# Kernel tuning notes

Measured on AMD Instinct MI355X. Metric: run time of the kernel, lower is better.

Reference implementation:

```python
import jax, jax.numpy as jnp
import numpy as np

BN_EPS = 1e-5


def setup_inputs() -> dict:
    key = jax.random.key(0)
    ks = jax.random.split(key, 12)
    N, K, C_IN, C_OUT = 50000, 16, 128, 128
    C2 = 2 * C_OUT
    return {
        "features": jax.random.normal(ks[0], (N, C_IN), dtype=jnp.float32),
        "neighbor_idx": jax.random.randint(ks[1], (N, K), 0, N, dtype=jnp.int64),
        "W1": jax.random.normal(ks[2], (C_IN, C2), dtype=jnp.float32) * 0.05,
        "b1": jax.random.normal(ks[3], (C2,), dtype=jnp.float32) * 0.05,
        "gamma": jax.random.uniform(ks[4], (C2,), dtype=jnp.float32, minval=0.5, maxval=1.5),
        "beta": jax.random.normal(ks[5], (C2,), dtype=jnp.float32) * 0.05,
        "run_mean": jax.random.normal(ks[6], (C2,), dtype=jnp.float32) * 0.05,
        "run_var": jax.random.uniform(ks[7], (C2,), dtype=jnp.float32, minval=0.5, maxval=1.5),
        "Ws": jax.random.normal(ks[8], (C2, C2), dtype=jnp.float32) * 0.05,
        "Wm": jax.random.normal(ks[9], (C2, C_OUT), dtype=jnp.float32) * 0.05,
        "bm": jax.random.normal(ks[10], (C_OUT,), dtype=jnp.float32) * 0.05,
    }


def reference(features, neighbor_idx, W1, b1, gamma, beta, run_mean, run_var, Ws, Wm, bm):
    # mlp1: Linear + ReLU (no BN)
    x = jax.nn.relu(features @ W1 + b1)                     # (N, 2C)
    # gather_neighbour: irregular index_select
    g = x[neighbor_idx]                                     # (N, k, 2C)
    # BatchNorm1d over channel dim (inference semantics, running stats)
    inv = gamma * jax.lax.rsqrt(run_var + BN_EPS)
    g = (g - run_mean) * inv + beta                         # (N, k, 2C)
    # AttentivePooling: per-neighbor score linear (no bias), softmax over k
    scores = jax.nn.softmax(g @ Ws, axis=1)                 # (N, k, 2C)
    feat = jnp.sum(scores * g, axis=1)                      # (N, 2C)
    return feat @ Wm + bm                                   # (N, C_out)
```

## Files before the change

kernel.cpp:

```cpp
#include <hip/hip_runtime.h>
#include <cstddef>

#define C_IN  128
#define C2    256
#define C_OUT 128
#define KNBR  16

typedef unsigned short u16;
typedef __attribute__((ext_vector_type(8))) short bf16x8;
typedef __attribute__((ext_vector_type(4))) float f32x4;

__device__ __forceinline__ float bf2f(u16 h) {
    return __uint_as_float(((unsigned int)h) << 16);
}
__device__ __forceinline__ u16 f2bf(float x) {
    unsigned int u = __float_as_uint(x);
    return (u16)((u + 0x7fffu + ((u >> 16) & 1u)) >> 16);
}

__global__ void prep_k(const float* __restrict__ W1, const float* __restrict__ Ws,
                       const float* __restrict__ Wm, u16* __restrict__ W1t,
                       u16* __restrict__ Wst, u16* __restrict__ Wmt)
{
    const int n = blockIdx.x, t = threadIdx.x;
    if (blockIdx.y == 0) {
        if (t < 128) W1t[n * 128 + t] = f2bf(W1[t * 256 + n]);
    } else if (blockIdx.y == 1) {
        Wst[n * 256 + t] = f2bf(Ws[t * 256 + n]);
    } else {
        if (n < 128) Wmt[n * 256 + t] = f2bf(Wm[t * 128 + n]);
    }
}

template<int MODE, bool A_BF16>
__global__ __launch_bounds__(256)
void mfma_gemm(const void* __restrict__ Ap, int lda,
               const u16* __restrict__ Bt,
               const float* __restrict__ bias, const float* __restrict__ gamma,
               const float* __restrict__ beta, const float* __restrict__ mean,
               const float* __restrict__ var,
               float* __restrict__ Cf, u16* __restrict__ packed,
               u16* __restrict__ xbn_c, int M, int Kd, int Nc)
{
    __shared__ u16 As[128][72];
    __shared__ u16 Bs[128][72];
    const int tid = threadIdx.x;
    const int w = tid >> 6, l = tid & 63, q = l >> 4, r = l & 15;
    const int wm = w & 1, wn = w >> 1;
    const int m0 = blockIdx.x * 128, n0 = blockIdx.y * 128;

    f32x4 acc[4][4] = {};

    for (int k0 = 0; k0 < Kd; k0 += 64) {
        if (A_BF16) {
            const u16* A = (const u16*)Ap;
            #pragma unroll
            for (int i = 0; i < 4; i++) {
                int idx = tid + i * 256;
                int row = idx >> 3, g = (idx & 7) * 8;
                int gm = m0 + row;
                uint4 v = make_uint4(0u, 0u, 0u, 0u);
                if (gm < M)
                    v = *(const uint4*)(A + (size_t)gm * lda + k0 + g);
                *(uint4*)&As[row][g] = v;
            }
        } else {
            const float* A = (const float*)Ap;
            #pragma unroll
            for (int i = 0; i < 8; i++) {
                int idx = tid + i * 256;
                int row = idx >> 4, g = (idx & 15) * 4;
                int gm = m0 + row;
                float4 v = make_float4(0.f, 0.f, 0.f, 0.f);
                if (gm < M)
                    v = *(const float4*)(A + (size_t)gm * lda + k0 + g);
                ushort4 h;
                h.x = f2bf(v.x); h.y = f2bf(v.y);
                h.z = f2bf(v.z); h.w = f2bf(v.w);
                *(ushort4*)&As[row][g] = h;
            }
        }
        #pragma unroll
        for (int i = 0; i < 4; i++) {
            int idx = tid + i * 256;
            int row = idx >> 3, g = (idx & 7) * 8;
            *(uint4*)&Bs[row][g] =
                *(const uint4*)(Bt + (size_t)(n0 + row) * Kd + k0 + g);
        }
        __syncthreads();

        #pragma unroll
        for (int h = 0; h < 2; h++) {
            bf16x8 af[4], bfr[4];
            #pragma unroll
            for (int i = 0; i < 4; i++)
                af[i] = *(const bf16x8*)&As[wm * 64 + i * 16 + r][h * 32 + q * 8];
            #pragma unroll
            for (int j = 0; j < 4; j++)
                bfr[j] = *(const bf16x8*)&Bs[wn * 64 + j * 16 + r][h * 32 + q * 8];
            #pragma unroll
            for (int i = 0; i < 4; i++)
                #pragma unroll
                for (int j = 0; j < 4; j++)
                    acc[i][j] = __builtin_amdgcn_mfma_f32_16x16x32_bf16(
                        af[i], bfr[j], acc[i][j], 0, 0, 0);
        }
        __syncthreads();
    }

    #pragma unroll
    for (int j = 0; j < 4; j++) {
        const int ch = n0 + wn * 64 + j * 16 + r;
        float bi = 0.f, be = 0.f, mu = 0.f, iv = 0.f, bo = 0.f;
        if (MODE == 1) {
            bi = bias[ch]; be = beta[ch]; mu = mean[ch];
            iv = gamma[ch] * rsqrtf(var[ch] + 1e-5f);
        }
        if (MODE == 2) bo = bias[ch];
        const int goff = (ch >> 2) * 8 + (ch & 3);
        #pragma unroll
        for (int i = 0; i < 4; i++) {
            const int mb = m0 + wm * 64 + i * 16 + q * 4;
            #pragma unroll
            for (int p = 0; p < 4; p++) {
                const int m = mb + p;
                if (m >= M) continue;
                float x = acc[i][j][p];
                if (MODE == 1) {
                    x = fmaxf(x + bi, 0.f);
                    x = (x - mu) * iv + be;
                    u16 hx = f2bf(x);
                    packed[(size_t)m * 512 + goff + 4] = hx;
                    xbn_c[(size_t)m * 256 + ch] = hx;
                } else if (MODE == 0) {
                    packed[(size_t)m * 512 + goff] = f2bf(__expf(x));
                } else {
                    Cf[(size_t)m * Nc + ch] = x + bo;
                }
            }
        }
    }
}

__global__ __launch_bounds__(256)
void gather_k(const u16* __restrict__ packed, const int* __restrict__ nidx,
              u16* __restrict__ featb, int N)
{
    __shared__ int rows[4 * KNBR];
    const int tid = threadIdx.x;
    const int p0 = blockIdx.x * 4;

    if (tid < 4 * KNBR) {
        int n = p0 + (tid >> 4);
        rows[tid] = (n < N) ? nidx[n * KNBR + (tid & 15)] : 0;
    }
    __syncthreads();

    const int w = tid >> 6;
    const int l = tid & 63;
    const int p = p0 + w;
    if (p >= N) return;

    uint4 v[KNBR];
    #pragma unroll
    for (int k = 0; k < KNBR; k++)
        v[k] = *(const uint4*)(packed + (size_t)rows[w * KNBR + k] * 512 + l * 8);

    float d0 = 0.f, d1 = 0.f, d2 = 0.f, d3 = 0.f;
    float u0 = 0.f, u1 = 0.f, u2 = 0.f, u3 = 0.f;
    #pragma unroll
    for (int k = 0; k < KNBR; k++) {
        float e0 = __uint_as_float(v[k].x << 16);
        float e1 = __uint_as_float(v[k].x & 0xffff0000u);
        float e2 = __uint_as_float(v[k].y << 16);
        float e3 = __uint_as_float(v[k].y & 0xffff0000u);
        float x0 = __uint_as_float(v[k].z << 16);
        float x1 = __uint_as_float(v[k].z & 0xffff0000u);
        float x2 = __uint_as_float(v[k].w << 16);
        float x3 = __uint_as_float(v[k].w & 0xffff0000u);
        d0 += e0; d1 += e1; d2 += e2; d3 += e3;
        u0 = fmaf(e0, x0, u0);
        u1 = fmaf(e1, x1, u1);
        u2 = fmaf(e2, x2, u2);
        u3 = fmaf(e3, x3, u3);
    }
    ushort4 o;
    o.x = f2bf(u0 / d0); o.y = f2bf(u1 / d1);
    o.z = f2bf(u2 / d2); o.w = f2bf(u3 / d3);
    *(ushort4*)(featb + (size_t)p * C2 + l * 4) = o;
}

extern "C" void kernel_launch(void* const* d_in, const int* in_sizes, int n_in,
                              void* d_out, int out_size, void* d_ws, size_t ws_size,
                              hipStream_t stream)
{
    const float* features = (const float*)d_in[0];
    const int*   nidx     = (const int*)d_in[1];
    const float* W1       = (const float*)d_in[2];
    const float* b1       = (const float*)d_in[3];
    const float* gamma    = (const float*)d_in[4];
    const float* beta     = (const float*)d_in[5];
    const float* mean     = (const float*)d_in[6];
    const float* var      = (const float*)d_in[7];
    const float* Ws       = (const float*)d_in[8];
    const float* Wm       = (const float*)d_in[9];
    const float* bm       = (const float*)d_in[10];
    float* out = (float*)d_out;

    const int N = in_sizes[0] / C_IN;

    u16* packed = (u16*)d_ws;
    u16* xbn_c  = packed + (size_t)N * 512;
    u16* W1t    = xbn_c + (size_t)N * 256;
    u16* Wst    = W1t + 256 * 128;
    u16* Wmt    = Wst + 256 * 256;
    u16* featb = (u16*)d_out;

    prep_k<<<dim3(256, 3), 256, 0, stream>>>(W1, Ws, Wm, W1t, Wst, Wmt);

    const int MT = (N + 127) / 128;

    mfma_gemm<1, false><<<dim3(MT, 2), 256, 0, stream>>>(
        features, C_IN, W1t, b1, gamma, beta, mean, var,
        nullptr, packed, xbn_c, N, C_IN, C2);
    mfma_gemm<0, true><<<dim3(MT, 2), 256, 0, stream>>>(
        xbn_c, C2, Wst, nullptr, nullptr, nullptr, nullptr, nullptr,
        nullptr, packed, nullptr, N, C2, C2);
    gather_k<<<(N + 3) / 4, 256, 0, stream>>>(packed, nidx, featb, N);
    mfma_gemm<2, true><<<dim3(MT, 1), 256, 0, stream>>>(
        featb, C2, Wmt, bm, nullptr, nullptr, nullptr, nullptr,
        out, nullptr, nullptr, N, C2, C_OUT);
}
```

Before: 292.9 us.

## Fuse mlp1 and score GEMMs into one kernel keeping activations in LDS

Merges the mlp1+BN GEMM and the score GEMM into a single kernel that keeps the BN-normalized tile in shared memory, removing the intermediate xbn_c buffer and one launch. The packed buffer layout changes from interleaved exp/x groups to separate halves, and the gather kernel loads two 8-byte chunks per neighbor accordingly. The fused kernel uses a large LDS footprint, lowering occupancy, and the gather's memory access becomes split into two smaller loads.

```diff
diff --git a/kernel.cpp b/kernel.cpp
--- a/kernel.cpp
+++ b/kernel.cpp
@@ -32,63 +32,164 @@
     }
 }
 
-template<int MODE, bool A_BF16>
 __global__ __launch_bounds__(256)
-void mfma_gemm(const void* __restrict__ Ap, int lda,
-               const u16* __restrict__ Bt,
-               const float* __restrict__ bias, const float* __restrict__ gamma,
-               const float* __restrict__ beta, const float* __restrict__ mean,
-               const float* __restrict__ var,
-               float* __restrict__ Cf, u16* __restrict__ packed,
-               u16* __restrict__ xbn_c, int M, int Kd, int Nc)
+void mlp_k(const float* __restrict__ F, const u16* __restrict__ W1t,
+           const u16* __restrict__ Wst,
+           const float* __restrict__ bias, const float* __restrict__ gamma,
+           const float* __restrict__ beta, const float* __restrict__ mean,
+           const float* __restrict__ var,
+           u16* __restrict__ packed, int N)
+{
+    __shared__ u16 As[128][136];
+    __shared__ u16 Bs[128][72];
+    __shared__ u16 xs[128][264];
+
+    const int tid = threadIdx.x;
+    const int w = tid >> 6, l = tid & 63, q = l >> 4, r = l & 15;
+    const int wm = w & 1, wn = w >> 1;
+    const int m0 = blockIdx.x * 128;
+
+    #pragma unroll
+    for (int i = 0; i < 16; i++) {
+        int idx = tid + i * 256;
+        int row = idx >> 5, c4 = (idx & 31) * 4;
+        int gm = m0 + row;
+        float4 v = make_float4(0.f, 0.f, 0.f, 0.f);
+        if (gm < N) v = *(const float4*)(F + (size_t)gm * C_IN + c4);
+        ushort4 h;
+        h.x = f2bf(v.x); h.y = f2bf(v.y); h.z = f2bf(v.z); h.w = f2bf(v.w);
+        *(ushort4*)&As[row][c4] = h;
+    }
+
+    #pragma unroll 1
+    for (int nh = 0; nh < 2; nh++) {
+        f32x4 acc[4][4] = {};
+        #pragma unroll 1
+        for (int k0 = 0; k0 < C_IN; k0 += 64) {
+            __syncthreads();
+            #pragma unroll
+            for (int i = 0; i < 4; i++) {
+                int idx = tid + i * 256;
+                int row = idx >> 3, g = (idx & 7) * 8;
+                *(uint4*)&Bs[row][g] = *(const uint4*)(
+                    W1t + (size_t)(nh * 128 + row) * C_IN + k0 + g);
+            }
+            __syncthreads();
+            #pragma unroll
+            for (int h = 0; h < 2; h++) {
+                bf16x8 af[4], bfr[4];
+                #pragma unroll
+                for (int i = 0; i < 4; i++)
+                    af[i] = *(const bf16x8*)&As[wm * 64 + i * 16 + r][k0 + h * 32 + q * 8];
+                #pragma unroll
+                for (int j = 0; j < 4; j++)
+                    bfr[j] = *(const bf16x8*)&Bs[wn * 64 + j * 16 + r][h * 32 + q * 8];
+                #pragma unroll
+                for (int i = 0; i < 4; i++)
+                    #pragma unroll
+                    for (int j = 0; j < 4; j++)
+                        acc[i][j] = __builtin_amdgcn_mfma_f32_16x16x32_bf16(
+                            af[i], bfr[j], acc[i][j], 0, 0, 0);
+            }
+        }
+        #pragma unroll
+        for (int j = 0; j < 4; j++) {
+            const int ch = nh * 128 + wn * 64 + j * 16 + r;
+            const float bi = bias[ch], be = beta[ch], mu = mean[ch];
+            const float iv = gamma[ch] * rsqrtf(var[ch] + 1e-5f);
+            #pragma unroll
+            for (int i = 0; i < 4; i++) {
+                const int mb = wm * 64 + i * 16 + q * 4;
+                #pragma unroll
+                for (int p = 0; p < 4; p++) {
+                    const int ml = mb + p;
+                    float x = fmaxf(acc[i][j][p] + bi, 0.f);
+                    x = (x - mu) * iv + be;
+                    u16 hx = f2bf(x);
+                    xs[ml][ch] = hx;
+                    if (m0 + ml < N)
+                        packed[(size_t)(m0 + ml) * 512 + 256 + ch] = hx;
+                }
+            }
+        }
+    }
+
+    #pragma unroll 1
+    for (int nh = 0; nh < 2; nh++) {
+        f32x4 acc[4][4] = {};
+        #pragma unroll 1
+        for (int k0 = 0; k0 < C2; k0 += 64) {
+            __syncthreads();
+            #pragma unroll
+            for (int i = 0; i < 4; i++) {
+                int idx = tid + i * 256;
+                int row = idx >> 3, g = (idx & 7) * 8;
+                *(uint4*)&Bs[row][g] = *(const uint4*)(
+                    Wst + (size_t)(nh * 128 + row) * C2 + k0 + g);
+            }
+            __syncthreads();
+            #pragma unroll
+            for (int h = 0; h < 2; h++) {
+                bf16x8 af[4], bfr[4];
+                #pragma unroll
+                for (int i = 0; i < 4; i++)
+                    af[i] = *(const bf16x8*)&xs[wm * 64 + i * 16 + r][k0 + h * 32 + q * 8];
+                #pragma unroll
+                for (int j = 0; j < 4; j++)
+                    bfr[j] = *(const bf16x8*)&Bs[wn * 64 + j * 16 + r][h * 32 + q * 8];
+                #pragma unroll
+                for (int i = 0; i < 4; i++)
+                    #pragma unroll
+                    for (int j = 0; j < 4; j++)
+                        acc[i][j] = __builtin_amdgcn_mfma_f32_16x16x32_bf16(
+                            af[i], bfr[j], acc[i][j], 0, 0, 0);
+            }
+        }
+        #pragma unroll
+        for (int j = 0; j < 4; j++) {
+            const int ch = nh * 128 + wn * 64 + j * 16 + r;
+            #pragma unroll
+            for (int i = 0; i < 4; i++) {
+                const int mb = wm * 64 + i * 16 + q * 4;
+                #pragma unroll
+                for (int p = 0; p < 4; p++) {
+                    const int ml = mb + p;
+                    if (m0 + ml < N)
+                        packed[(size_t)(m0 + ml) * 512 + ch] =
+                            f2bf(__expf(acc[i][j][p]));
+                }
+            }
+        }
+    }
+}
+
+__global__ __launch_bounds__(256)
+void out_gemm(const u16* __restrict__ A, const u16* __restrict__ Bt,
+              const float* __restrict__ bias, float* __restrict__ Cf, int N)
 {
     __shared__ u16 As[128][72];
     __shared__ u16 Bs[128][72];
     const int tid = threadIdx.x;
     const int w = tid >> 6, l = tid & 63, q = l >> 4, r = l & 15;
     const int wm = w & 1, wn = w >> 1;
-    const int m0 = blockIdx.x * 128, n0 = blockIdx.y * 128;
+    const int m0 = blockIdx.x * 128;
 
     f32x4 acc[4][4] = {};
 
-    for (int k0 = 0; k0 < Kd; k0 += 64) {
-        if (A_BF16) {
-            const u16* A = (const u16*)Ap;
-            #pragma unroll
-            for (int i = 0; i < 4; i++) {
-                int idx = tid + i * 256;
-                int row = idx >> 3, g = (idx & 7) * 8;
-                int gm = m0 + row;
-                uint4 v = make_uint4(0u, 0u, 0u, 0u);
-                if (gm < M)
-                    v = *(const uint4*)(A + (size_t)gm * lda + k0 + g);
-                *(uint4*)&As[row][g] = v;
-            }
-        } else {
-            const float* A = (const float*)Ap;
-            #pragma unroll
-            for (int i = 0; i < 8; i++) {
-                int idx = tid + i * 256;
-                int row = idx >> 4, g = (idx & 15) * 4;
-                int gm = m0 + row;
-                float4 v = make_float4(0.f, 0.f, 0.f, 0.f);
-                if (gm < M)
-                    v = *(const float4*)(A + (size_t)gm * lda + k0 + g);
-                ushort4 h;
-                h.x = f2bf(v.x); h.y = f2bf(v.y);
-                h.z = f2bf(v.z); h.w = f2bf(v.w);
-                *(ushort4*)&As[row][g] = h;
-            }
-        }
+    #pragma unroll 1
+    for (int k0 = 0; k0 < C2; k0 += 64) {
         #pragma unroll
         for (int i = 0; i < 4; i++) {
             int idx = tid + i * 256;
             int row = idx >> 3, g = (idx & 7) * 8;
-            *(uint4*)&Bs[row][g] =
-                *(const uint4*)(Bt + (size_t)(n0 + row) * Kd + k0 + g);
+            int gm = m0 + row;
+            uint4 v = make_uint4(0u, 0u, 0u, 0u);
+            if (gm < N) v = *(const uint4*)(A + (size_t)gm * C2 + k0 + g);
+            *(uint4*)&As[row][g] = v;
+            *(uint4*)&Bs[row][g] = *(const uint4*)(
+                Bt + (size_t)row * C2 + k0 + g);
         }
         __syncthreads();
-
         #pragma unroll
         for (int h = 0; h < 2; h++) {
             bf16x8 af[4], bfr[4];
@@ -110,33 +211,15 @@
 
     #pragma unroll
     for (int j = 0; j < 4; j++) {
-        const int ch = n0 + wn * 64 + j * 16 + r;
-        float bi = 0.f, be = 0.f, mu = 0.f, iv = 0.f, bo = 0.f;
-        if (MODE == 1) {
-            bi = bias[ch]; be = beta[ch]; mu = mean[ch];
-            iv = gamma[ch] * rsqrtf(var[ch] + 1e-5f);
-        }
-        if (MODE == 2) bo = bias[ch];
-        const int goff = (ch >> 2) * 8 + (ch & 3);
+        const int ch = wn * 64 + j * 16 + r;
+        const float bo = bias[ch];
         #pragma unroll
         for (int i = 0; i < 4; i++) {
             const int mb = m0 + wm * 64 + i * 16 + q * 4;
             #pragma unroll
             for (int p = 0; p < 4; p++) {
                 const int m = mb + p;
-                if (m >= M) continue;
-                float x = acc[i][j][p];
-                if (MODE == 1) {
-                    x = fmaxf(x + bi, 0.f);
-                    x = (x - mu) * iv + be;
-                    u16 hx = f2bf(x);
-                    packed[(size_t)m * 512 + goff + 4] = hx;
-                    xbn_c[(size_t)m * 256 + ch] = hx;
-                } else if (MODE == 0) {
-                    packed[(size_t)m * 512 + goff] = f2bf(__expf(x));
-                } else {
-                    Cf[(size_t)m * Nc + ch] = x + bo;
-                }
+                if (m < N) Cf[(size_t)m * C_OUT + ch] = acc[i][j][p] + bo;
             }
         }
     }
@@ -161,28 +244,25 @@
     const int p = p0 + w;
     if (p >= N) return;
 
-    uint4 v[KNBR];
+    ushort4 eh[KNBR], xh[KNBR];
     #pragma unroll
-    for (int k = 0; k < KNBR; k++)
-        v[k] = *(const uint4*)(packed + (size_t)rows[w * KNBR + k] * 512 + l * 8);
+    for (int k = 0; k < KNBR; k++) {
+        const size_t base = (size_t)rows[w * KNBR + k] * 512;
+        eh[k] = *(const ushort4*)(packed + base + l * 4);
+        xh[k] = *(const ushort4*)(packed + base + 256 + l * 4);
+    }
 
     float d0 = 0.f, d1 = 0.f, d2 = 0.f, d3 = 0.f;
     float u0 = 0.f, u1 = 0.f, u2 = 0.f, u3 = 0.f;
     #pragma unroll
     for (int k = 0; k < KNBR; k++) {
-        float e0 = __uint_as_float(v[k].x << 16);
-        float e1 = __uint_as_float(v[k].x & 0xffff0000u);
-        float e2 = __uint_as_float(v[k].y << 16);
-        float e3 = __uint_as_float(v[k].y & 0xffff0000u);
-        float x0 = __uint_as_float(v[k].z << 16);
-        float x1 = __uint_as_float(v[k].z & 0xffff0000u);
-        float x2 = __uint_as_float(v[k].w << 16);
-        float x3 = __uint_as_float(v[k].w & 0xffff0000u);
+        float e0 = bf2f(eh[k].x), e1 = bf2f(eh[k].y);
+        float e2 = bf2f(eh[k].z), e3 = bf2f(eh[k].w);
         d0 += e0; d1 += e1; d2 += e2; d3 += e3;
-        u0 = fmaf(e0, x0, u0);
-        u1 = fmaf(e1, x1, u1);
-        u2 = fmaf(e2, x2, u2);
-        u3 = fmaf(e3, x3, u3);
+        u0 = fmaf(e0, bf2f(xh[k].x), u0);
+        u1 = fmaf(e1, bf2f(xh[k].y), u1);
+        u2 = fmaf(e2, bf2f(xh[k].z), u2);
+        u3 = fmaf(e3, bf2f(xh[k].w), u3);
     }
     ushort4 o;
     o.x = f2bf(u0 / d0); o.y = f2bf(u1 / d1);
@@ -210,8 +290,7 @@
     const int N = in_sizes[0] / C_IN;
 
     u16* packed = (u16*)d_ws;
-    u16* xbn_c  = packed + (size_t)N * 512;
-    u16* W1t    = xbn_c + (size_t)N * 256;
+    u16* W1t    = packed + (size_t)N * 512;
     u16* Wst    = W1t + 256 * 128;
     u16* Wmt    = Wst + 256 * 256;
     u16* featb = (u16*)d_out;
@@ -220,14 +299,8 @@
 
     const int MT = (N + 127) / 128;
 
-    mfma_gemm<1, false><<<dim3(MT, 2), 256, 0, stream>>>(
-        features, C_IN, W1t, b1, gamma, beta, mean, var,
-        nullptr, packed, xbn_c, N, C_IN, C2);
-    mfma_gemm<0, true><<<dim3(MT, 2), 256, 0, stream>>>(
-        xbn_c, C2, Wst, nullptr, nullptr, nullptr, nullptr, nullptr,
-        nullptr, packed, nullptr, N, C2, C2);
+    mlp_k<<<MT, 256, 0, stream>>>(features, W1t, Wst, b1, gamma, beta,
+                                  mean, var, packed, N);
     gather_k<<<(N + 3) / 4, 256, 0, stream>>>(packed, nidx, featb, N);
-    mfma_gemm<2, true><<<dim3(MT, 1), 256, 0, stream>>>(
-        featb, C2, Wmt, bm, nullptr, nullptr, nullptr, nullptr,
-        out, nullptr, nullptr, N, C2, C_OUT);
-}
+    out_gemm<<<MT, 256, 0, stream>>>(featb, Wmt, bm, out, N);
+}
```

Result: faster. 268.2 us (-8.5%).
